# Kernel optimization log

Hardware: AMD Instinct MI355X
Metric: run time of the kernel (lower is better)

The kernel has to match this reference:

```python
import jax, jax.numpy as jnp
import numpy as np

B, L, D, DEG = 32, 1024, 512, 8
E = B * L * DEG  # 262144 edges total
N = B * L


def setup_inputs() -> dict:
    key = jax.random.key(0)
    ks = jax.random.split(key, 8)
    text_feature = jax.random.normal(ks[0], (B, L, D), jnp.float32)
    # edge list per sample (torch.nonzero(edge_matrix[i]) equivalent), offset by b*L like PyG batching
    src_local = jax.random.randint(ks[1], (E,), 0, L, jnp.int32)
    dst_local = jax.random.randint(ks[2], (E,), 0, L, jnp.int32)
    boff = (jnp.arange(E, dtype=jnp.int32) // (E // B)) * L
    edge_src = src_local + boff
    edge_dst = dst_local + boff
    s = 1.0 / np.sqrt(D)
    W1 = jax.random.uniform(ks[3], (D, D), jnp.float32, -s, s)   # node Linear
    b1 = jax.random.uniform(ks[4], (D,), jnp.float32, -s, s)
    gamma = jnp.ones((D,), jnp.float32)      # BatchNorm1d weight
    beta = jnp.zeros((D,), jnp.float32)      # BatchNorm1d bias
    run_mean = jnp.zeros((D,), jnp.float32)  # BN running stats (eval mode)
    run_var = jnp.ones((D,), jnp.float32)
    alpha1 = jnp.array(0.25, jnp.float32)    # PReLU (node MLP)
    Wg = jax.random.uniform(ks[5], (D, D), jnp.float32, -s, s)   # GCNConv lin (bias=False)
    bg = jnp.zeros((D,), jnp.float32)        # GCNConv bias
    alpha2 = jnp.array(0.25, jnp.float32)    # PReLU (after GCN)
    return {"text_feature": text_feature, "edge_src": edge_src, "edge_dst": edge_dst,
            "W1": W1, "b1": b1, "gamma": gamma, "beta": beta,
            "run_mean": run_mean, "run_var": run_var, "alpha1": alpha1,
            "Wg": Wg, "bg": bg, "alpha2": alpha2}


def reference(text_feature, edge_src, edge_dst, W1, b1, gamma, beta,
              run_mean, run_var, alpha1, Wg, bg, alpha2):
    Bs, Ls, Ds = text_feature.shape
    Nn = Bs * Ls
    xf = text_feature.reshape(Nn, Ds)
    # node MLP: Linear -> BatchNorm1d (eval) -> PReLU
    h = xf @ W1 + b1
    h = (h - run_mean) * jax.lax.rsqrt(run_var + 1e-5) * gamma + beta
    h = jnp.where(h >= 0, h, alpha1 * h)
    # GCNConv: add self loops, symmetric degree norm, gather->scatter-add, + bias
    nodes = jnp.arange(Nn, dtype=edge_src.dtype)
    src = jnp.concatenate([edge_src, nodes])
    dst = jnp.concatenate([edge_dst, nodes])
    deg = jnp.zeros((Nn,), h.dtype).at[dst].add(1.0)  # in-degree incl. self loop, >= 1
    dinv = jax.lax.rsqrt(deg)
    xw = h @ Wg                               # [N, D]
    msg = (xw * dinv[:, None])[src]           # gather D^{-1/2}-scaled messages [E+N, D]
    agg = jnp.zeros_like(xw).at[dst].add(msg) * dinv[:, None]
    g = agg + bg
    g = jnp.where(g >= 0, g, alpha2 * g)      # PReLU
    g = g.reshape(Bs, Ls, Ds)
    # F.normalize(p=2, dim=2) + residual (original input)
    g = g / jnp.clip(jnp.linalg.norm(g, axis=2, keepdims=True), 1e-12)
    return g + text_feature
```

## Files before the change

kernel.cpp:

```cpp
#include <hip/hip_runtime.h>
#include <math.h>

#define DD    512
#define NN    32768
#define EE    262144

typedef float f32x4 __attribute__((ext_vector_type(4)));
typedef __bf16 bf16x8 __attribute__((ext_vector_type(8)));

#define AS1 __attribute__((address_space(1)))
#define AS3 __attribute__((address_space(3)))

__global__ void k_zero(int* __restrict__ cnt) {
    int i = blockIdx.x * 256 + threadIdx.x;
    if (i < NN) cnt[i] = 0;
}

__global__ void k_count(const int* __restrict__ dst, int* __restrict__ cnt) {
    int e = blockIdx.x * 256 + threadIdx.x;
    if (e < EE) atomicAdd(&cnt[dst[e]], 1);
}

__global__ __launch_bounds__(1024) void k_scan(
    const int* __restrict__ cnt, int* __restrict__ offs,
    int* __restrict__ cursor, float* __restrict__ dinv)
{
    __shared__ int part[1024];
    int t = threadIdx.x;
    int base = t * 32;
    int local[32];
    int s = 0;
#pragma unroll
    for (int i = 0; i < 32; ++i) { local[i] = s; s += cnt[base + i]; }
    part[t] = s;
    __syncthreads();
    for (int off = 1; off < 1024; off <<= 1) {
        int v = (t >= off) ? part[t - off] : 0;
        __syncthreads();
        part[t] += v;
        __syncthreads();
    }
    int prev = (t == 0) ? 0 : part[t - 1];
#pragma unroll
    for (int i = 0; i < 32; ++i) {
        int o = prev + local[i];
        offs[base + i] = o;
        cursor[base + i] = o;
        dinv[base + i] = rsqrtf((float)cnt[base + i] + 1.0f);
    }
    if (t == 1023) offs[NN] = part[1023];
}

__global__ void k_fill(const int* __restrict__ src, const int* __restrict__ dst,
                       int* __restrict__ cursor, int* __restrict__ csr) {
    int e = blockIdx.x * 256 + threadIdx.x;
    if (e < EE) {
        int d = dst[e];
        int p = atomicAdd(&cursor[d], 1);
        csr[p] = src[e];
    }
}

__global__ __launch_bounds__(256) void k_wt(const float* __restrict__ W1, const float* __restrict__ Wg,
                                            __bf16* __restrict__ W1t, __bf16* __restrict__ Wgt) {
    __shared__ float tile[32][33];
    const float* W = blockIdx.z ? Wg : W1;
    __bf16* Wt = blockIdx.z ? Wgt : W1t;
    int x0 = blockIdx.x * 32;
    int y0 = blockIdx.y * 32;
    int tx = threadIdx.x;
    for (int j = threadIdx.y; j < 32; j += 8)
        tile[j][tx] = W[(size_t)(y0 + j) * DD + x0 + tx];
    __syncthreads();
    for (int j = threadIdx.y; j < 32; j += 8)
        Wt[(size_t)(x0 + j) * DD + y0 + tx] = (__bf16)tile[tx][j];
}

template <int MODE>
__global__ __launch_bounds__(512, 2) void k_gemm_w(
    const void* __restrict__ Ap,
    const __bf16* __restrict__ Wt,
    __bf16* __restrict__ Cout,
    const float* __restrict__ bias,
    const float* __restrict__ gamma, const float* __restrict__ beta,
    const float* __restrict__ mean, const float* __restrict__ var,
    const float* __restrict__ alphap)
{
    __shared__ __bf16 slab[2][16384];

    const int t    = threadIdx.x;
    const int lane = t & 63;
    const int wv   = t >> 6;
    const int l15  = lane & 15;
    const int lhi  = lane >> 4;
    const int work = ((blockIdx.x & 7) << 6) + (blockIdx.x >> 3);
    const int nsl  = work & 1;
    const int mb   = work >> 1;
    const int mbase   = mb * 128;
    const int colbase = nsl * 256 + wv * 32;

    bf16x8 wf[2][16];
#pragma unroll
    for (int C = 0; C < 2; ++C)
#pragma unroll
        for (int kf = 0; kf < 16; ++kf) {
            int col = colbase + C * 16 + l15;
            wf[C][kf] = *(const bf16x8*)(Wt + (size_t)col * DD + kf * 32 + lhi * 8);
        }

    float s0 = 0, s1 = 0, t0 = 0, t1 = 0, al = 0;
    if constexpr (MODE == 1) {
        int c0 = colbase + l15, c1 = c0 + 16;
        float r0 = rsqrtf(var[c0] + 1e-5f), r1 = rsqrtf(var[c1] + 1e-5f);
        s0 = gamma[c0] * r0;  s1 = gamma[c1] * r1;
        t0 = (bias[c0] - mean[c0]) * s0 + beta[c0];
        t1 = (bias[c1] - mean[c1]) * s1 + beta[c1];
        al = alphap[0];
    }

    float4 fa[4][2];

    auto loadA1 = [&](int mt) {
        const float* A = (const float*)Ap;
#pragma unroll
        for (int q = 0; q < 4; ++q) {
            int d = q * 512 + t;
            int kf = d >> 7, r = (d >> 2) & 31, s = d & 3;
            int c = kf * 4 + (s ^ ((r >> 1) & 3));
            const float* g = A + (size_t)(mbase + mt * 32 + r) * DD + c * 8;
            fa[q][0] = *(const float4*)g;
            fa[q][1] = *(const float4*)(g + 4);
        }
    };
    auto writeA1 = [&](int bb) {
#pragma unroll
        for (int q = 0; q < 4; ++q) {
            int d = q * 512 + t;
            bf16x8 o;
            o[0] = (__bf16)fa[q][0].x; o[1] = (__bf16)fa[q][0].y;
            o[2] = (__bf16)fa[q][0].z; o[3] = (__bf16)fa[q][0].w;
            o[4] = (__bf16)fa[q][1].x; o[5] = (__bf16)fa[q][1].y;
            o[6] = (__bf16)fa[q][1].z; o[7] = (__bf16)fa[q][1].w;
            *(bf16x8*)&slab[bb][(size_t)d * 8] = o;
        }
    };
    auto stage2 = [&](int bb, int mt) {
        const __bf16* A = (const __bf16*)Ap;
#pragma unroll
        for (int q = 0; q < 4; ++q) {
            int d  = q * 512 + wv * 64 + lane;
            int kf = d >> 7, r = (d >> 2) & 31, s = d & 3;
            int c  = kf * 4 + (s ^ ((r >> 1) & 3));
            const __bf16* g = A + (size_t)(mbase + mt * 32 + r) * DD + c * 8;
            __builtin_amdgcn_global_load_lds(
                (const AS1 unsigned int*)g,
                (AS3 unsigned int*)(&slab[bb][(size_t)(q * 512 + wv * 64) * 8]), 16, 0, 0);
        }
    };

    if constexpr (MODE == 1) { loadA1(0); writeA1(0); }
    else                     { stage2(0, 0); }
    __syncthreads();

#pragma unroll
    for (int mt = 0; mt < 4; ++mt) {
        const int cur = mt & 1, nxt = cur ^ 1;

        if (mt < 3) {
            if constexpr (MODE == 1) loadA1(mt + 1);
            else                     stage2(nxt, mt + 1);
        }

        f32x4 acc[2][2] = {};
        const __bf16* sl = &slab[cur][0];
#pragma unroll
        for (int kf = 0; kf < 16; ++kf) {
            int r0 = l15, r1 = 16 + l15;
            int sA = lhi ^ ((r0 >> 1) & 3);
            int sB = lhi ^ ((r1 >> 1) & 3);
            bf16x8 a0 = *(const bf16x8*)&sl[(kf * 128 + r0 * 4 + sA) * 8];
            bf16x8 a1 = *(const bf16x8*)&sl[(kf * 128 + r1 * 4 + sB) * 8];
            acc[0][0] = __builtin_amdgcn_mfma_f32_16x16x32_bf16(a0, wf[0][kf], acc[0][0], 0, 0, 0);
            acc[0][1] = __builtin_amdgcn_mfma_f32_16x16x32_bf16(a0, wf[1][kf], acc[0][1], 0, 0, 0);
            acc[1][0] = __builtin_amdgcn_mfma_f32_16x16x32_bf16(a1, wf[0][kf], acc[1][0], 0, 0, 0);
            acc[1][1] = __builtin_amdgcn_mfma_f32_16x16x32_bf16(a1, wf[1][kf], acc[1][1], 0, 0, 0);
        }

#pragma unroll
        for (int R = 0; R < 2; ++R)
#pragma unroll
            for (int C = 0; C < 2; ++C) {
                int col  = colbase + C * 16 + l15;
                int rowb = mbase + mt * 32 + R * 16 + (lhi << 2);
#pragma unroll
                for (int j = 0; j < 4; ++j) {
                    float x = acc[R][C][j];
                    if constexpr (MODE == 1) {
                        float ss = C ? s1 : s0, tt = C ? t1 : t0;
                        x = x * ss + tt;
                        x = (x >= 0.0f) ? x : al * x;
                    }
                    Cout[(size_t)(rowb + j) * DD + col] = (__bf16)x;
                }
            }

        if constexpr (MODE == 1) {
            if (mt < 3) writeA1(nxt);
        }

        __syncthreads();
    }
}

__global__ __launch_bounds__(256) void k_gather_final(
    const int* __restrict__ offs, const int* __restrict__ csr,
    const __bf16* __restrict__ xws, const float* __restrict__ dinv,
    const float* __restrict__ bg, const float* __restrict__ alpha2,
    const float* __restrict__ text, float* __restrict__ out)
{
    int blk = blockIdx.x;
    int sb  = ((blk & 7) << 10) + (blk >> 3);
    int wave = threadIdx.x >> 6;
    int lane = threadIdx.x & 63;
    int node = sb * 4 + wave;
    int c = lane * 8;
    int beg = offs[node], end = offs[node + 1];
    int ne = end - beg;

    float dn = dinv[node];
    bf16x8 sv = *(const bf16x8*)(xws + (size_t)node * DD + c);
    float a[8];
#pragma unroll
    for (int i = 0; i < 8; ++i) a[i] = dn * (float)sv[i];

    int k = 0;
    for (; k + 4 <= ne; k += 4) {
        int s0 = csr[beg + k + 0];
        int s1 = csr[beg + k + 1];
        int s2 = csr[beg + k + 2];
        int s3 = csr[beg + k + 3];
        float d0 = dinv[s0], d1 = dinv[s1], d2 = dinv[s2], d3 = dinv[s3];
        bf16x8 v0 = *(const bf16x8*)(xws + (size_t)s0 * DD + c);
        bf16x8 v1 = *(const bf16x8*)(xws + (size_t)s1 * DD + c);
        bf16x8 v2 = *(const bf16x8*)(xws + (size_t)s2 * DD + c);
        bf16x8 v3 = *(const bf16x8*)(xws + (size_t)s3 * DD + c);
#pragma unroll
        for (int i = 0; i < 8; ++i)
            a[i] += d0 * (float)v0[i] + d1 * (float)v1[i] + d2 * (float)v2[i] + d3 * (float)v3[i];
    }
    for (; k < ne; ++k) {
        int s = csr[beg + k];
        float ds_ = dinv[s];
        bf16x8 v = *(const bf16x8*)(xws + (size_t)s * DD + c);
#pragma unroll
        for (int i = 0; i < 8; ++i) a[i] += ds_ * (float)v[i];
    }

    float al = alpha2[0];
    float g[8];
    float ss = 0.0f;
#pragma unroll
    for (int i = 0; i < 8; ++i) {
        float x = a[i] * dn + bg[c + i];
        x = (x >= 0.0f) ? x : al * x;
        g[i] = x;
        ss += x * x;
    }
#pragma unroll
    for (int off = 1; off < 64; off <<= 1) ss += __shfl_xor(ss, off, 64);
    float inv = 1.0f / fmaxf(sqrtf(ss), 1e-12f);

    size_t base = (size_t)node * DD + c;
    float4 t0 = *(const float4*)&text[base];
    float4 t1 = *(const float4*)&text[base + 4];
    float4 o0, o1;
    o0.x = g[0] * inv + t0.x; o0.y = g[1] * inv + t0.y;
    o0.z = g[2] * inv + t0.z; o0.w = g[3] * inv + t0.w;
    o1.x = g[4] * inv + t1.x; o1.y = g[5] * inv + t1.y;
    o1.z = g[6] * inv + t1.z; o1.w = g[7] * inv + t1.w;
    *(float4*)&out[base]     = o0;
    *(float4*)&out[base + 4] = o1;
}

extern "C" void kernel_launch(void* const* d_in, const int* in_sizes, int n_in,
                              void* d_out, int out_size, void* d_ws, size_t ws_size,
                              hipStream_t stream) {
    const float* text   = (const float*)d_in[0];
    const int*   esrc   = (const int*)d_in[1];
    const int*   edst   = (const int*)d_in[2];
    const float* W1     = (const float*)d_in[3];
    const float* b1     = (const float*)d_in[4];
    const float* gamma  = (const float*)d_in[5];
    const float* beta   = (const float*)d_in[6];
    const float* rmean  = (const float*)d_in[7];
    const float* rvar   = (const float*)d_in[8];
    const float* alpha1 = (const float*)d_in[9];
    const float* Wg     = (const float*)d_in[10];
    const float* bg     = (const float*)d_in[11];
    const float* alpha2 = (const float*)d_in[12];
    float* out = (float*)d_out;

    char* p = (char*)d_ws;
    auto alloc = [&](size_t bytes) { char* r = p; p += (bytes + 255) & ~(size_t)255; return r; };
    int*    cnt     = (int*)alloc((size_t)NN * 4);
    int*    offs    = (int*)alloc((size_t)(NN + 1) * 4);
    int*    cursor  = (int*)alloc((size_t)NN * 4);
    float*  dinv    = (float*)alloc((size_t)NN * 4);
    int*    csr     = (int*)alloc((size_t)EE * 4);
    __bf16* W1t     = (__bf16*)alloc((size_t)DD * DD * 2);
    __bf16* Wgt     = (__bf16*)alloc((size_t)DD * DD * 2);
    __bf16* h_bf    = (__bf16*)alloc((size_t)NN * DD * 2);
    __bf16* xws     = (__bf16*)alloc((size_t)NN * DD * 2);

    k_zero<<<NN / 256, 256, 0, stream>>>(cnt);
    k_count<<<EE / 256, 256, 0, stream>>>(edst, cnt);
    k_scan<<<1, 1024, 0, stream>>>(cnt, offs, cursor, dinv);
    k_fill<<<EE / 256, 256, 0, stream>>>(esrc, edst, cursor, csr);

    k_wt<<<dim3(16, 16, 2), dim3(32, 8), 0, stream>>>(W1, Wg, W1t, Wgt);

    k_gemm_w<1><<<512, 512, 0, stream>>>(text, W1t, h_bf, b1, gamma, beta, rmean, rvar, alpha1);

    k_gemm_w<2><<<512, 512, 0, stream>>>(h_bf, Wgt, xws, nullptr, nullptr, nullptr, nullptr, nullptr, nullptr);

    k_gather_final<<<NN / 4, 256, 0, stream>>>(offs, csr, xws, dinv, bg, alpha2, text, out);
}
```

Measured before the change: 158.3 us.

## Double the GEMM row tile and add three-stage async LDS pipeline

Each GEMM block now handles 256 rows instead of 128, cutting the grid from 512 to 256 blocks so the register-resident W fragments are loaded half as often. The MODE 2 path gains a triple-buffered global_load_lds pipeline with explicit vmcnt waits, so loads run two tiles ahead. Both paths replace __syncthreads with a bare s_barrier plus manual waitcnts, and the MFMA loop runs at raised wave priority. The risks are lower occupancy and fewer blocks than CUs (256 blocks on the mi355x), plus more LDS per block in MODE 2.

```diff
diff --git a/kernel.cpp b/kernel.cpp
--- a/kernel.cpp
+++ b/kernel.cpp
@@ -86,17 +86,17 @@
     const float* __restrict__ mean, const float* __restrict__ var,
     const float* __restrict__ alphap)
 {
-    __shared__ __bf16 slab[2][16384];
+    __shared__ __bf16 slab[MODE == 1 ? 2 : 3][16384];
 
     const int t    = threadIdx.x;
     const int lane = t & 63;
     const int wv   = t >> 6;
     const int l15  = lane & 15;
     const int lhi  = lane >> 4;
-    const int work = ((blockIdx.x & 7) << 6) + (blockIdx.x >> 3);
+    const int work = ((blockIdx.x & 7) << 5) + (blockIdx.x >> 3);
     const int nsl  = work & 1;
     const int mb   = work >> 1;
-    const int mbase   = mb * 128;
+    const int mbase   = mb * 256;
     const int colbase = nsl * 256 + wv * 32;
 
     bf16x8 wf[2][16];
@@ -158,21 +158,31 @@
         }
     };
 
-    if constexpr (MODE == 1) { loadA1(0); writeA1(0); }
-    else                     { stage2(0, 0); }
-    __syncthreads();
-
-#pragma unroll
-    for (int mt = 0; mt < 4; ++mt) {
-        const int cur = mt & 1, nxt = cur ^ 1;
-
-        if (mt < 3) {
-            if constexpr (MODE == 1) loadA1(mt + 1);
-            else                     stage2(nxt, mt + 1);
+    if constexpr (MODE == 1) {
+        loadA1(0); writeA1(0);
+        asm volatile("s_waitcnt lgkmcnt(0)" ::: "memory");
+        __builtin_amdgcn_s_barrier();
+    } else {
+        stage2(0, 0);
+        stage2(1, 1);
+        asm volatile("s_waitcnt vmcnt(4)" ::: "memory");
+        __builtin_amdgcn_s_barrier();
+    }
+    asm volatile("" ::: "memory");
+
+#pragma unroll
+    for (int mt = 0; mt < 8; ++mt) {
+        const int cur = (MODE == 1) ? (mt & 1) : (mt % 3);
+
+        if constexpr (MODE == 1) {
+            if (mt < 7) loadA1(mt + 1);
+        } else {
+            if (mt < 6) stage2((mt + 2) % 3, mt + 2);
         }
 
         f32x4 acc[2][2] = {};
         const __bf16* sl = &slab[cur][0];
+        __builtin_amdgcn_s_setprio(1);
 #pragma unroll
         for (int kf = 0; kf < 16; ++kf) {
             int r0 = l15, r1 = 16 + l15;
@@ -185,6 +195,7 @@
             acc[1][0] = __builtin_amdgcn_mfma_f32_16x16x32_bf16(a1, wf[0][kf], acc[1][0], 0, 0, 0);
             acc[1][1] = __builtin_amdgcn_mfma_f32_16x16x32_bf16(a1, wf[1][kf], acc[1][1], 0, 0, 0);
         }
+        __builtin_amdgcn_s_setprio(0);
 
 #pragma unroll
         for (int R = 0; R < 2; ++R)
@@ -205,10 +216,17 @@
             }
 
         if constexpr (MODE == 1) {
-            if (mt < 3) writeA1(nxt);
-        }
-
-        __syncthreads();
+            if (mt < 7) {
+                writeA1(mt & 1 ? 0 : 1);
+                asm volatile("s_waitcnt lgkmcnt(0)" ::: "memory");
+                __builtin_amdgcn_s_barrier();
+            }
+        } else {
+            if (mt < 6)      asm volatile("s_waitcnt vmcnt(4)" ::: "memory");
+            else if (mt == 6) asm volatile("s_waitcnt vmcnt(0)" ::: "memory");
+            if (mt < 7) __builtin_amdgcn_s_barrier();
+        }
+        asm volatile("" ::: "memory");
     }
 }
 
@@ -319,9 +337,9 @@
 
     k_wt<<<dim3(16, 16, 2), dim3(32, 8), 0, stream>>>(W1, Wg, W1t, Wgt);
 
-    k_gemm_w<1><<<512, 512, 0, stream>>>(text, W1t, h_bf, b1, gamma, beta, rmean, rvar, alpha1);
-
-    k_gemm_w<2><<<512, 512, 0, stream>>>(h_bf, Wgt, xws, nullptr, nullptr, nullptr, nullptr, nullptr, nullptr);
+    k_gemm_w<1><<<256, 512, 0, stream>>>(text, W1t, h_bf, b1, gamma, beta, rmean, rvar, alpha1);
+
+    k_gemm_w<2><<<256, 512, 0, stream>>>(h_bf, Wgt, xws, nullptr, nullptr, nullptr, nullptr, nullptr, nullptr);
 
     k_gather_final<<<NN / 4, 256, 0, stream>>>(offs, csr, xws, dinv, bg, alpha2, text, out);
 }
```

Measured after the change: 151.9 us. 1.04x faster.

## Double rows per GEMM block and load second GEMM's A directly into registers

Applied to the files above, without the earlier changes.

Both GEMMs now use 256 blocks, each covering 256 rows instead of 128, so each block's register-resident weight fragments are reused across twice as many row tiles. The second GEMM drops its LDS staging and instead loads bf16 A fragments straight from global memory into registers, with a two-deep software prefetch interleaved with the MFMAs. This removes LDS traffic and barriers from GEMM2 and halves the repeated weight loads. The cost is fewer blocks on the device, which may leave some CUs idle, and more exposed global-load latency in GEMM2.

```diff
diff --git a/kernel.cpp b/kernel.cpp
--- a/kernel.cpp
+++ b/kernel.cpp
@@ -76,9 +76,8 @@
         Wt[(size_t)(x0 + j) * DD + y0 + tx] = (__bf16)tile[tx][j];
 }
 
-template <int MODE>
-__global__ __launch_bounds__(512, 2) void k_gemm_w(
-    const void* __restrict__ Ap,
+__global__ __launch_bounds__(512, 2) void k_gemm1(
+    const float* __restrict__ A,
     const __bf16* __restrict__ Wt,
     __bf16* __restrict__ Cout,
     const float* __restrict__ bias,
@@ -93,10 +92,10 @@
     const int wv   = t >> 6;
     const int l15  = lane & 15;
     const int lhi  = lane >> 4;
-    const int work = ((blockIdx.x & 7) << 6) + (blockIdx.x >> 3);
+    const int work = ((blockIdx.x & 7) << 5) + (blockIdx.x >> 3);
     const int nsl  = work & 1;
     const int mb   = work >> 1;
-    const int mbase   = mb * 128;
+    const int mbase   = mb * 256;
     const int colbase = nsl * 256 + wv * 32;
 
     bf16x8 wf[2][16];
@@ -108,8 +107,8 @@
             wf[C][kf] = *(const bf16x8*)(Wt + (size_t)col * DD + kf * 32 + lhi * 8);
         }
 
-    float s0 = 0, s1 = 0, t0 = 0, t1 = 0, al = 0;
-    if constexpr (MODE == 1) {
+    float s0, s1, t0, t1, al;
+    {
         int c0 = colbase + l15, c1 = c0 + 16;
         float r0 = rsqrtf(var[c0] + 1e-5f), r1 = rsqrtf(var[c1] + 1e-5f);
         s0 = gamma[c0] * r0;  s1 = gamma[c1] * r1;
@@ -121,7 +120,6 @@
     float4 fa[4][2];
 
     auto loadA1 = [&](int mt) {
-        const float* A = (const float*)Ap;
 #pragma unroll
         for (int q = 0; q < 4; ++q) {
             int d = q * 512 + t;
@@ -144,32 +142,15 @@
             *(bf16x8*)&slab[bb][(size_t)d * 8] = o;
         }
     };
-    auto stage2 = [&](int bb, int mt) {
-        const __bf16* A = (const __bf16*)Ap;
-#pragma unroll
-        for (int q = 0; q < 4; ++q) {
-            int d  = q * 512 + wv * 64 + lane;
-            int kf = d >> 7, r = (d >> 2) & 31, s = d & 3;
-            int c  = kf * 4 + (s ^ ((r >> 1) & 3));
-            const __bf16* g = A + (size_t)(mbase + mt * 32 + r) * DD + c * 8;
-            __builtin_amdgcn_global_load_lds(
-                (const AS1 unsigned int*)g,
-                (AS3 unsigned int*)(&slab[bb][(size_t)(q * 512 + wv * 64) * 8]), 16, 0, 0);
-        }
-    };
-
-    if constexpr (MODE == 1) { loadA1(0); writeA1(0); }
-    else                     { stage2(0, 0); }
+
+    loadA1(0); writeA1(0);
     __syncthreads();
 
 #pragma unroll
-    for (int mt = 0; mt < 4; ++mt) {
+    for (int mt = 0; mt < 8; ++mt) {
         const int cur = mt & 1, nxt = cur ^ 1;
 
-        if (mt < 3) {
-            if constexpr (MODE == 1) loadA1(mt + 1);
-            else                     stage2(nxt, mt + 1);
-        }
+        if (mt < 7) loadA1(mt + 1);
 
         f32x4 acc[2][2] = {};
         const __bf16* sl = &slab[cur][0];
@@ -192,23 +173,90 @@
             for (int C = 0; C < 2; ++C) {
                 int col  = colbase + C * 16 + l15;
                 int rowb = mbase + mt * 32 + R * 16 + (lhi << 2);
+                float ss = C ? s1 : s0, tt = C ? t1 : t0;
 #pragma unroll
                 for (int j = 0; j < 4; ++j) {
-                    float x = acc[R][C][j];
-                    if constexpr (MODE == 1) {
-                        float ss = C ? s1 : s0, tt = C ? t1 : t0;
-                        x = x * ss + tt;
-                        x = (x >= 0.0f) ? x : al * x;
-                    }
+                    float x = acc[R][C][j] * ss + tt;
+                    x = (x >= 0.0f) ? x : al * x;
                     Cout[(size_t)(rowb + j) * DD + col] = (__bf16)x;
                 }
             }
 
-        if constexpr (MODE == 1) {
-            if (mt < 3) writeA1(nxt);
-        }
-
+        if (mt < 7) writeA1(nxt);
         __syncthreads();
+    }
+}
+
+__global__ __launch_bounds__(512) void k_gemm2_bf(
+    const __bf16* __restrict__ A,
+    const __bf16* __restrict__ Wt,
+    __bf16* __restrict__ Cout)
+{
+    const int t    = threadIdx.x;
+    const int lane = t & 63;
+    const int wv   = t >> 6;
+    const int l15  = lane & 15;
+    const int lhi  = lane >> 4;
+    const int work = ((blockIdx.x & 7) << 5) + (blockIdx.x >> 3);
+    const int nsl  = work & 1;
+    const int mb   = work >> 1;
+    const int mbase   = mb * 256;
+    const int colbase = nsl * 256 + wv * 32;
+
+    bf16x8 wf[2][16];
+#pragma unroll
+    for (int C = 0; C < 2; ++C)
+#pragma unroll
+        for (int kf = 0; kf < 16; ++kf) {
+            int col = colbase + C * 16 + l15;
+            wf[C][kf] = *(const bf16x8*)(Wt + (size_t)col * DD + kf * 32 + lhi * 8);
+        }
+
+    const __bf16* pA0 = A + (size_t)(mbase + l15) * DD + lhi * 8;
+    const __bf16* pA1 = pA0 + 16 * DD;
+
+#pragma unroll
+    for (int mt = 0; mt < 8; ++mt) {
+        const __bf16* q0 = pA0 + (size_t)mt * 32 * DD;
+        const __bf16* q1 = pA1 + (size_t)mt * 32 * DD;
+
+        f32x4 acc[2][2] = {};
+
+        bf16x8 a0e = *(const bf16x8*)(q0);
+        bf16x8 a1e = *(const bf16x8*)(q1);
+        bf16x8 a0o = *(const bf16x8*)(q0 + 32);
+        bf16x8 a1o = *(const bf16x8*)(q1 + 32);
+
+#pragma unroll
+        for (int kf = 0; kf < 16; kf += 2) {
+            acc[0][0] = __builtin_amdgcn_mfma_f32_16x16x32_bf16(a0e, wf[0][kf], acc[0][0], 0, 0, 0);
+            acc[0][1] = __builtin_amdgcn_mfma_f32_16x16x32_bf16(a0e, wf[1][kf], acc[0][1], 0, 0, 0);
+            acc[1][0] = __builtin_amdgcn_mfma_f32_16x16x32_bf16(a1e, wf[0][kf], acc[1][0], 0, 0, 0);
+            acc[1][1] = __builtin_amdgcn_mfma_f32_16x16x32_bf16(a1e, wf[1][kf], acc[1][1], 0, 0, 0);
+            if (kf + 2 < 16) {
+                a0e = *(const bf16x8*)(q0 + (kf + 2) * 32);
+                a1e = *(const bf16x8*)(q1 + (kf + 2) * 32);
+            }
+            acc[0][0] = __builtin_amdgcn_mfma_f32_16x16x32_bf16(a0o, wf[0][kf + 1], acc[0][0], 0, 0, 0);
+            acc[0][1] = __builtin_amdgcn_mfma_f32_16x16x32_bf16(a0o, wf[1][kf + 1], acc[0][1], 0, 0, 0);
+            acc[1][0] = __builtin_amdgcn_mfma_f32_16x16x32_bf16(a1o, wf[0][kf + 1], acc[1][0], 0, 0, 0);
+            acc[1][1] = __builtin_amdgcn_mfma_f32_16x16x32_bf16(a1o, wf[1][kf + 1], acc[1][1], 0, 0, 0);
+            if (kf + 3 < 16) {
+                a0o = *(const bf16x8*)(q0 + (kf + 3) * 32);
+                a1o = *(const bf16x8*)(q1 + (kf + 3) * 32);
+            }
+        }
+
+#pragma unroll
+        for (int R = 0; R < 2; ++R)
+#pragma unroll
+            for (int C = 0; C < 2; ++C) {
+                int col  = colbase + C * 16 + l15;
+                int rowb = mbase + mt * 32 + R * 16 + (lhi << 2);
+#pragma unroll
+                for (int j = 0; j < 4; ++j)
+                    Cout[(size_t)(rowb + j) * DD + col] = (__bf16)acc[R][C][j];
+            }
     }
 }
 
@@ -319,9 +367,9 @@
 
     k_wt<<<dim3(16, 16, 2), dim3(32, 8), 0, stream>>>(W1, Wg, W1t, Wgt);
 
-    k_gemm_w<1><<<512, 512, 0, stream>>>(text, W1t, h_bf, b1, gamma, beta, rmean, rvar, alpha1);
-
-    k_gemm_w<2><<<512, 512, 0, stream>>>(h_bf, Wgt, xws, nullptr, nullptr, nullptr, nullptr, nullptr, nullptr);
+    k_gemm1<<<256, 512, 0, stream>>>(text, W1t, h_bf, b1, gamma, beta, rmean, rvar, alpha1);
+
+    k_gemm2_bf<<<256, 512, 0, stream>>>(h_bf, Wgt, xws);
 
     k_gather_final<<<NN / 4, 256, 0, stream>>>(offs, csr, xws, dinv, bg, alpha2, text, out);
 }
```

After: 185.1 us. +16.9%, slower.

## Fuse the two GEMMs into one kernel keeping hidden activations in LDS

Applied to the files above, without the earlier changes.

Merges the node-MLP GEMM and the GCN weight GEMM into a single kernel. Each block computes a full 128x512 tile of h, keeps it in a 128KB LDS buffer, then multiplies it by Wg, so the bf16 h intermediate never goes to global memory. In exchange the grid drops to 256 blocks, LDS use grows to about 160KB so only one block fits per CU, and the weight fragments are reloaded for every pass. A-tile loading is now single-buffered with extra barriers.

```diff
diff --git a/kernel.cpp b/kernel.cpp
--- a/kernel.cpp
+++ b/kernel.cpp
@@ -76,52 +76,42 @@
         Wt[(size_t)(x0 + j) * DD + y0 + tx] = (__bf16)tile[tx][j];
 }
 
-template <int MODE>
-__global__ __launch_bounds__(512, 2) void k_gemm_w(
-    const void* __restrict__ Ap,
-    const __bf16* __restrict__ Wt,
-    __bf16* __restrict__ Cout,
-    const float* __restrict__ bias,
+__global__ __launch_bounds__(512, 2) void k_fused(
+    const float* __restrict__ A,
+    const __bf16* __restrict__ W1t,
+    const __bf16* __restrict__ Wgt,
+    __bf16* __restrict__ Xout,
+    const float* __restrict__ b1,
     const float* __restrict__ gamma, const float* __restrict__ beta,
     const float* __restrict__ mean, const float* __restrict__ var,
     const float* __restrict__ alphap)
 {
-    __shared__ __bf16 slab[2][16384];
+    __shared__ __bf16 hbuf[65536];
+    __shared__ __bf16 slab[16384];
 
     const int t    = threadIdx.x;
     const int lane = t & 63;
     const int wv   = t >> 6;
     const int l15  = lane & 15;
     const int lhi  = lane >> 4;
-    const int work = ((blockIdx.x & 7) << 6) + (blockIdx.x >> 3);
-    const int nsl  = work & 1;
-    const int mb   = work >> 1;
-    const int mbase   = mb * 128;
-    const int colbase = nsl * 256 + wv * 32;
-
-    bf16x8 wf[2][16];
-#pragma unroll
-    for (int C = 0; C < 2; ++C)
-#pragma unroll
-        for (int kf = 0; kf < 16; ++kf) {
-            int col = colbase + C * 16 + l15;
-            wf[C][kf] = *(const bf16x8*)(Wt + (size_t)col * DD + kf * 32 + lhi * 8);
-        }
-
-    float s0 = 0, s1 = 0, t0 = 0, t1 = 0, al = 0;
-    if constexpr (MODE == 1) {
-        int c0 = colbase + l15, c1 = c0 + 16;
-        float r0 = rsqrtf(var[c0] + 1e-5f), r1 = rsqrtf(var[c1] + 1e-5f);
-        s0 = gamma[c0] * r0;  s1 = gamma[c1] * r1;
-        t0 = (bias[c0] - mean[c0]) * s0 + beta[c0];
-        t1 = (bias[c1] - mean[c1]) * s1 + beta[c1];
-        al = alphap[0];
-    }
+    const int work = ((blockIdx.x & 7) << 5) + (blockIdx.x >> 3);
+    const int mbase = work * 128;
+
+    float sc[2][2], tc[2][2];
+    const float al = alphap[0];
+#pragma unroll
+    for (int p = 0; p < 2; ++p)
+#pragma unroll
+        for (int C = 0; C < 2; ++C) {
+            int c = p * 256 + wv * 32 + C * 16 + l15;
+            float r = rsqrtf(var[c] + 1e-5f);
+            sc[p][C] = gamma[c] * r;
+            tc[p][C] = (b1[c] - mean[c]) * sc[p][C] + beta[c];
+        }
 
     float4 fa[4][2];
 
     auto loadA1 = [&](int mt) {
-        const float* A = (const float*)Ap;
 #pragma unroll
         for (int q = 0; q < 4; ++q) {
             int d = q * 512 + t;
@@ -132,7 +122,7 @@
             fa[q][1] = *(const float4*)(g + 4);
         }
     };
-    auto writeA1 = [&](int bb) {
+    auto writeA1 = [&]() {
 #pragma unroll
         for (int q = 0; q < 4; ++q) {
             int d = q * 512 + t;
@@ -141,74 +131,104 @@
             o[2] = (__bf16)fa[q][0].z; o[3] = (__bf16)fa[q][0].w;
             o[4] = (__bf16)fa[q][1].x; o[5] = (__bf16)fa[q][1].y;
             o[6] = (__bf16)fa[q][1].z; o[7] = (__bf16)fa[q][1].w;
-            *(bf16x8*)&slab[bb][(size_t)d * 8] = o;
+            *(bf16x8*)&slab[(size_t)d * 8] = o;
         }
     };
-    auto stage2 = [&](int bb, int mt) {
-        const __bf16* A = (const __bf16*)Ap;
-#pragma unroll
-        for (int q = 0; q < 4; ++q) {
-            int d  = q * 512 + wv * 64 + lane;
-            int kf = d >> 7, r = (d >> 2) & 31, s = d & 3;
-            int c  = kf * 4 + (s ^ ((r >> 1) & 3));
-            const __bf16* g = A + (size_t)(mbase + mt * 32 + r) * DD + c * 8;
-            __builtin_amdgcn_global_load_lds(
-                (const AS1 unsigned int*)g,
-                (AS3 unsigned int*)(&slab[bb][(size_t)(q * 512 + wv * 64) * 8]), 16, 0, 0);
-        }
-    };
-
-    if constexpr (MODE == 1) { loadA1(0); writeA1(0); }
-    else                     { stage2(0, 0); }
+
+    loadA1(0); writeA1();
     __syncthreads();
 
 #pragma unroll
     for (int mt = 0; mt < 4; ++mt) {
-        const int cur = mt & 1, nxt = cur ^ 1;
-
+        if (mt < 3) loadA1(mt + 1);
+
+#pragma unroll
+        for (int pass = 0; pass < 2; ++pass) {
+            bf16x8 wf[2][16];
+#pragma unroll
+            for (int C = 0; C < 2; ++C)
+#pragma unroll
+                for (int kf = 0; kf < 16; ++kf) {
+                    int col = pass * 256 + wv * 32 + C * 16 + l15;
+                    wf[C][kf] = *(const bf16x8*)(W1t + (size_t)col * DD + kf * 32 + lhi * 8);
+                }
+
+            f32x4 acc[2][2] = {};
+#pragma unroll
+            for (int kf = 0; kf < 16; ++kf) {
+                int r0 = l15, r1 = 16 + l15;
+                int sA = lhi ^ ((r0 >> 1) & 3);
+                int sB = lhi ^ ((r1 >> 1) & 3);
+                bf16x8 a0 = *(const bf16x8*)&slab[(kf * 128 + r0 * 4 + sA) * 8];
+                bf16x8 a1 = *(const bf16x8*)&slab[(kf * 128 + r1 * 4 + sB) * 8];
+                acc[0][0] = __builtin_amdgcn_mfma_f32_16x16x32_bf16(a0, wf[0][kf], acc[0][0], 0, 0, 0);
+                acc[0][1] = __builtin_amdgcn_mfma_f32_16x16x32_bf16(a0, wf[1][kf], acc[0][1], 0, 0, 0);
+                acc[1][0] = __builtin_amdgcn_mfma_f32_16x16x32_bf16(a1, wf[0][kf], acc[1][0], 0, 0, 0);
+                acc[1][1] = __builtin_amdgcn_mfma_f32_16x16x32_bf16(a1, wf[1][kf], acc[1][1], 0, 0, 0);
+            }
+
+#pragma unroll
+            for (int R = 0; R < 2; ++R)
+#pragma unroll
+                for (int C = 0; C < 2; ++C) {
+                    int k = pass * 256 + wv * 32 + C * 16 + l15;
+                    int kf2 = k >> 5, kc = (k >> 3) & 3, kb = k & 7;
+#pragma unroll
+                    for (int j = 0; j < 4; ++j) {
+                        int row = mt * 32 + R * 16 + (lhi << 2) + j;
+                        float x = acc[R][C][j] * sc[pass][C] + tc[pass][C];
+                        x = (x >= 0.0f) ? x : al * x;
+                        int s2 = kc ^ ((row >> 1) & 3);
+                        hbuf[(size_t)(kf2 * 512 + row * 4 + s2) * 8 + kb] = (__bf16)x;
+                    }
+                }
+        }
+
+        __syncthreads();
         if (mt < 3) {
-            if constexpr (MODE == 1) loadA1(mt + 1);
-            else                     stage2(nxt, mt + 1);
-        }
-
-        f32x4 acc[2][2] = {};
-        const __bf16* sl = &slab[cur][0];
+            writeA1();
+            __syncthreads();
+        }
+    }
+
+#pragma unroll
+    for (int pass = 0; pass < 2; ++pass) {
+        bf16x8 wg[2][16];
+#pragma unroll
+        for (int C = 0; C < 2; ++C)
+#pragma unroll
+            for (int kf = 0; kf < 16; ++kf) {
+                int col = pass * 256 + wv * 32 + C * 16 + l15;
+                wg[C][kf] = *(const bf16x8*)(Wgt + (size_t)col * DD + kf * 32 + lhi * 8);
+            }
+
+        f32x4 acc2[8][2] = {};
 #pragma unroll
         for (int kf = 0; kf < 16; ++kf) {
-            int r0 = l15, r1 = 16 + l15;
-            int sA = lhi ^ ((r0 >> 1) & 3);
-            int sB = lhi ^ ((r1 >> 1) & 3);
-            bf16x8 a0 = *(const bf16x8*)&sl[(kf * 128 + r0 * 4 + sA) * 8];
-            bf16x8 a1 = *(const bf16x8*)&sl[(kf * 128 + r1 * 4 + sB) * 8];
-            acc[0][0] = __builtin_amdgcn_mfma_f32_16x16x32_bf16(a0, wf[0][kf], acc[0][0], 0, 0, 0);
-            acc[0][1] = __builtin_amdgcn_mfma_f32_16x16x32_bf16(a0, wf[1][kf], acc[0][1], 0, 0, 0);
-            acc[1][0] = __builtin_amdgcn_mfma_f32_16x16x32_bf16(a1, wf[0][kf], acc[1][0], 0, 0, 0);
-            acc[1][1] = __builtin_amdgcn_mfma_f32_16x16x32_bf16(a1, wf[1][kf], acc[1][1], 0, 0, 0);
-        }
-
-#pragma unroll
-        for (int R = 0; R < 2; ++R)
+            bf16x8 af[8];
+#pragma unroll
+            for (int rg = 0; rg < 8; ++rg) {
+                int r = rg * 16 + l15;
+                int s = lhi ^ ((r >> 1) & 3);
+                af[rg] = *(const bf16x8*)&hbuf[(size_t)(kf * 512 + r * 4 + s) * 8];
+            }
+#pragma unroll
+            for (int rg = 0; rg < 8; ++rg) {
+                acc2[rg][0] = __builtin_amdgcn_mfma_f32_16x16x32_bf16(af[rg], wg[0][kf], acc2[rg][0], 0, 0, 0);
+                acc2[rg][1] = __builtin_amdgcn_mfma_f32_16x16x32_bf16(af[rg], wg[1][kf], acc2[rg][1], 0, 0, 0);
+            }
+        }
+
+#pragma unroll
+        for (int rg = 0; rg < 8; ++rg)
 #pragma unroll
             for (int C = 0; C < 2; ++C) {
-                int col  = colbase + C * 16 + l15;
-                int rowb = mbase + mt * 32 + R * 16 + (lhi << 2);
-#pragma unroll
-                for (int j = 0; j < 4; ++j) {
-                    float x = acc[R][C][j];
-                    if constexpr (MODE == 1) {
-                        float ss = C ? s1 : s0, tt = C ? t1 : t0;
-                        x = x * ss + tt;
-                        x = (x >= 0.0f) ? x : al * x;
-                    }
-                    Cout[(size_t)(rowb + j) * DD + col] = (__bf16)x;
-                }
-            }
-
-        if constexpr (MODE == 1) {
-            if (mt < 3) writeA1(nxt);
-        }
-
-        __syncthreads();
+                int col  = pass * 256 + wv * 32 + C * 16 + l15;
+                int rowb = mbase + rg * 16 + (lhi << 2);
+#pragma unroll
+                for (int j = 0; j < 4; ++j)
+                    Xout[(size_t)(rowb + j) * DD + col] = (__bf16)acc2[rg][C][j];
+            }
     }
 }
 
@@ -309,7 +329,6 @@
     int*    csr     = (int*)alloc((size_t)EE * 4);
     __bf16* W1t     = (__bf16*)alloc((size_t)DD * DD * 2);
     __bf16* Wgt     = (__bf16*)alloc((size_t)DD * DD * 2);
-    __bf16* h_bf    = (__bf16*)alloc((size_t)NN * DD * 2);
     __bf16* xws     = (__bf16*)alloc((size_t)NN * DD * 2);
 
     k_zero<<<NN / 256, 256, 0, stream>>>(cnt);
@@ -319,9 +338,7 @@
 
     k_wt<<<dim3(16, 16, 2), dim3(32, 8), 0, stream>>>(W1, Wg, W1t, Wgt);
 
-    k_gemm_w<1><<<512, 512, 0, stream>>>(text, W1t, h_bf, b1, gamma, beta, rmean, rvar, alpha1);
-
-    k_gemm_w<2><<<512, 512, 0, stream>>>(h_bf, Wgt, xws, nullptr, nullptr, nullptr, nullptr, nullptr, nullptr);
+    k_fused<<<256, 512, 0, stream>>>(text, W1t, Wgt, xws, b1, gamma, beta, rmean, rvar, alpha1);
 
     k_gather_final<<<NN / 4, 256, 0, stream>>>(offs, csr, xws, dinv, bg, alpha2, text, out);
 }
```

Result: slower. 172.7 us (+9.1%).
